# Kernel tuning notes

Measured on AMD Instinct MI355X. Metric: run time of the kernel, lower is better.

Reference implementation:

```python
import jax, jax.numpy as jnp
import numpy as np

C_LOGIT = 10.0  # logit clipping constant C from __init__
NEG_INF = -1e9


def setup_inputs() -> dict:
    key = jax.random.key(0)
    ks = jax.random.split(key, 12)
    B, S, E, H = 128, 1024, 128, 128
    sE = 1.0 / np.sqrt(E)
    s2E = 1.0 / np.sqrt(2 * E)
    return {
        "node_context": jnp.zeros((1,), jnp.float32),   # unused: low-decoder results are discarded
        "original_data": jnp.zeros((1,), jnp.float32),  # unused
        "cell_context": jax.random.normal(ks[0], (B, S, E), jnp.float32),
        "high_mask": jnp.zeros((B, S), jnp.float32),
        "low_mask": jnp.zeros((1,), jnp.float32),       # unused
        # learned parameters
        "init_w": jax.random.uniform(ks[1], (2 * E,), jnp.float32, -1.0, 1.0),
        "Wc": jax.random.uniform(ks[2], (E, E), jnp.float32, -sE, sE),    # h_context_embed
        "bc": jax.random.uniform(ks[3], (E,), jnp.float32, -sE, sE),
        "Wv": jax.random.uniform(ks[4], (2 * E, E), jnp.float32, -s2E, s2E),  # v_weight_embed
        "bv": jax.random.uniform(ks[5], (E,), jnp.float32, -s2E, s2E),
        "W_ref": jax.random.uniform(ks[6], (E, H), jnp.float32, -sE, sE),  # pointer target proj
        "W_q": jax.random.uniform(ks[7], (E, H), jnp.float32, -sE, sE),    # pointer query proj
        "v": jax.random.uniform(ks[8], (H,), jnp.float32, -1.0 / np.sqrt(H), 1.0 / np.sqrt(H)),
    }


def reference(node_context, original_data, cell_context, high_mask, low_mask,
              init_w, Wc, bc, Wv, bv, W_ref, W_q, v):
    B, S, E = cell_context.shape
    h_bar = jnp.mean(cell_context, axis=1) @ Wc + bc            # [B, E]
    ref = jnp.einsum('bse,eh->bsh', cell_context, W_ref)        # [B, S, H] (loop-invariant)
    q0 = h_bar + (init_w @ Wv + bv)                             # [B, E]
    mask0 = high_mask.at[:, 0].set(1.0)                         # start node masked
    base_key = jax.random.key(42)

    def step(carry, i):
        query, mask, init_h = carry
        q = query @ W_q                                         # [B, H]
        u = C_LOGIT * jnp.tanh(jnp.einsum('bsh,h->bs', jnp.tanh(ref + q[:, None, :]), v))
        logits = jnp.where(mask > 0, NEG_INF, u)                # [B, S]
        k = jax.random.fold_in(base_key, i)
        idx = jax.random.categorical(k, logits)                 # [B] sampled next node
        logp = jnp.take_along_axis(jax.nn.log_softmax(logits, -1), idx[:, None], 1)[:, 0]
        mask = mask.at[jnp.arange(B), idx].set(1.0)             # Environment.update_state
        h = jnp.take_along_axis(cell_context, idx[:, None, None], 1)[:, 0, :]  # gather emb
        init_h = jnp.where(i == 0, h, init_h)                   # frozen after first step
        query = h_bar + jnp.concatenate([init_h, h], axis=-1) @ Wv + bv
        return (query, mask, init_h), (logp, idx)

    init = (q0, mask0, jnp.zeros((B, E), cell_context.dtype))
    _, (logps, idxs) = jax.lax.scan(step, init, jnp.arange(S - 1))
    # original returns (stack(log_probs, 1), stack(idx, 1))
    return logps.T, idxs.T
```

## Files before the change

kernel.cpp:

```cpp
#include <hip/hip_runtime.h>
#include <hip/hip_bf16.h>
#include <stdint.h>

#pragma clang fp contract(off)

#define Bn 128
#define Sn 1024
#define En 128
#define NSTEP 1023
#define REQ_WS ((size_t)Bn * 128 * Sn * 4)

__device__ __forceinline__ uint2 threefry2x32(uint32_t k0, uint32_t k1,
                                              uint32_t x0, uint32_t x1) {
  uint32_t ks2 = k0 ^ k1 ^ 0x1BD11BDAu;
  x0 += k0; x1 += k1;
#define TFR(r) { x0 += x1; x1 = (x1 << (r)) | (x1 >> (32 - (r))); x1 ^= x0; }
  TFR(13) TFR(15) TFR(26) TFR(6)
  x0 += k1;  x1 += ks2 + 1u;
  TFR(17) TFR(29) TFR(16) TFR(24)
  x0 += ks2; x1 += k0 + 2u;
  TFR(13) TFR(15) TFR(26) TFR(6)
  x0 += k0;  x1 += k1 + 3u;
  TFR(17) TFR(29) TFR(16) TFR(24)
  x0 += k1;  x1 += ks2 + 4u;
  TFR(13) TFR(15) TFR(26) TFR(6)
  x0 += ks2; x1 += k0 + 5u;
#undef TFR
  return make_uint2(x0, x1);
}

__device__ __forceinline__ float xla_tanh(float x) {
#pragma clang fp contract(off)
  float cx = fmaxf(-7.90531110763549805f, fminf(x, 7.90531110763549805f));
  float x2 = cx * cx;
  float nu = -2.76076847742355e-16f;
  nu = x2 * nu + 2.00018790482477e-13f;
  nu = x2 * nu + -8.60467152213735e-11f;
  nu = x2 * nu + 5.12229709037114e-08f;
  nu = x2 * nu + 1.48572235717979e-05f;
  nu = x2 * nu + 6.37261928875436e-04f;
  nu = x2 * nu + 4.89352455891786e-03f;
  nu = cx * nu;
  float de = 1.19825839466702e-06f;
  de = x2 * de + 1.18534705686654e-04f;
  de = x2 * de + 2.26843463243900e-03f;
  de = x2 * de + 4.89352518554385e-03f;
  float r = nu / de;
  return (fabsf(x) < 0.0004f) ? x : r;
}

__device__ __forceinline__ float cephes_logf(float x) {
#pragma clang fp contract(off)
  uint32_t ix = __float_as_uint(x);
  int e = (int)(ix >> 23) - 126;
  float m = __uint_as_float((ix & 0x007FFFFFu) | 0x3F000000u);
  if (m < 0.70710678118654752440f) { e -= 1; m = m + m; }
  float xm = m - 1.0f;
  float z = xm * xm;
  float y = 7.0376836292e-2f;
  y = y * xm + -1.1514610310e-1f;
  y = y * xm + 1.1676998740e-1f;
  y = y * xm + -1.2420140846e-1f;
  y = y * xm + 1.4249322787e-1f;
  y = y * xm + -1.6668057665e-1f;
  y = y * xm + 2.0000714765e-1f;
  y = y * xm + -2.4999993993e-1f;
  y = y * xm + 3.3333331174e-1f;
  y = y * xm;
  y = y * z;
  float fe = (float)e;
  y = y + fe * -2.12194440e-4f;
  y = y - 0.5f * z;
  float res = xm + y;
  res = res + fe * 0.693359375f;
  return res;
}

__device__ __forceinline__ float cephes_expf(float x) {
#pragma clang fp contract(off)
  x = fminf(fmaxf(x, -88.3762626647949f), 88.3762626647950f);
  float fx = x * 1.44269504088896341f + 0.5f;
  fx = floorf(fx);
  x = x - fx * 0.693359375f;
  x = x - fx * -2.12194440e-4f;
  float z = x * x;
  float y = 1.9875691500e-4f;
  y = y * x + 1.3981999507e-3f;
  y = y * x + 8.3334519073e-3f;
  y = y * x + 4.1665795894e-2f;
  y = y * x + 1.6666665459e-1f;
  y = y * x + 5.0000001201e-1f;
  y = y * z + x;
  y = y + 1.0f;
  return ldexpf(y, (int)fx);
}

__device__ __forceinline__ uint32_t f32_orderable(float f) {
  uint32_t b = __float_as_uint(f);
  return (b & 0x80000000u) ? ~b : (b | 0x80000000u);
}

__global__ void k_mark(float* out, float val) { out[0] = val; }

__global__ __launch_bounds__(256) void k_ref(const float* __restrict__ cc,
    const float* __restrict__ W_ref, float* __restrict__ refT) {
#pragma clang fp contract(off)
  int b = blockIdx.y, s0 = blockIdx.x * 128, t = threadIdx.x;
  __shared__ float tile[128 * 129];
  const float* src = cc + ((size_t)b * Sn + s0) * En;
  for (int i = t; i < 128 * 128; i += 256) {
    int sl = i >> 7, e = i & 127;
    tile[sl * 129 + e] = src[i];
  }
  __syncthreads();
  for (int i = t; i < 128 * 128; i += 256) {
    int sl = i >> 7, h = i & 127;
    float acc = 0.0f;
    for (int e = 0; e < En; ++e)
      acc = acc + tile[sl * 129 + e] * W_ref[e * 128 + h];
    refT[((size_t)b * Sn + (s0 + sl)) * 128 + h] = acc;
  }
}

__global__ __launch_bounds__(1024) void k_decode(
    const float* __restrict__ cc, const float* __restrict__ high_mask,
    const float* __restrict__ init_w, const float* __restrict__ Wc,
    const float* __restrict__ bc, const float* __restrict__ Wv,
    const float* __restrict__ bv, const float* __restrict__ W_q,
    const float* __restrict__ v, const float* __restrict__ refT,
    float* __restrict__ out, int half) {
#pragma clang fp contract(off)
  const int b = blockIdx.x, tid = threadIdx.x;
  const int lane = tid & 63, wid = tid >> 6;
  const int hsel = tid & 1;
  __shared__ __align__(16) float wq_s[128 * 128];
  __shared__ __align__(16) float wvhi_s[128 * 128];
  __shared__ __align__(16) float mean_s[128], q_s[128], query_s[128], hbar_s[128];
  __shared__ __align__(16) float v_s[128], bv_s[128], cvec[256], dlow_s[128];
  __shared__ float uv[1024];
  __shared__ unsigned short list_s[1024];
  __shared__ unsigned long long wkey[16];
  __shared__ float wsum[16];
  __shared__ int n_s, p_s;
  __shared__ uint32_t key_s[2];

  for (int j = tid; j < 128 * 128; j += 1024) wq_s[j] = W_q[j];
  for (int j = tid; j < 128 * 128; j += 1024) wvhi_s[j] = Wv[128 * 128 + j];
  if (tid < 128) {
    float acc = 0.0f;
    const float* base = cc + (size_t)b * Sn * En + tid;
    for (int s = 0; s < Sn; ++s) acc = acc + base[(size_t)s * En];
    mean_s[tid] = acc / 1024.0f;
  }
  if (tid == 512) {
    int n = 0;
    for (int s = 0; s < Sn; ++s) {
      bool masked = (s == 0) || (high_mask[(size_t)b * Sn + s] > 0.0f);
      if (!masked) list_s[n++] = (unsigned short)s;
    }
    n_s = n;
  }
  __syncthreads();
  if (tid < 128) {
    float hb = 0.0f;
    for (int e = 0; e < 128; ++e) hb = hb + mean_s[e] * Wc[e * 128 + tid];
    hb = hb + bc[tid];
    float wd = 0.0f;
    for (int k = 0; k < 256; ++k) wd = wd + init_w[k] * Wv[k * 128 + tid];
    wd = wd + bv[tid];
    hbar_s[tid] = hb;
    query_s[tid] = hb + wd;
    v_s[tid] = v[tid];
    bv_s[tid] = bv[tid];
  }
  __syncthreads();

  const float* refb = refT + (size_t)b * Sn * 128;
  const float4* q4 = (const float4*)q_s;
  const float4* v4 = (const float4*)v_s;

  for (int i = 0; i < NSTEP; ++i) {
    const int n = n_s;
    if (tid < 128) {
      float acc = 0.0f;
#pragma unroll 8
      for (int k = 0; k < 128; ++k) acc = acc + query_s[k] * wq_s[k * 128 + tid];
      q_s[tid] = acc;
    } else if (tid == 512) {
      uint2 kk2 = threefry2x32(0u, 42u, 0u, (uint32_t)i);
      key_s[0] = kk2.x; key_s[1] = kk2.y;
    }
    __syncthreads();

    const int npass = (2 * n + 1023) >> 10;
    unsigned long long kk = 0ull;
    float ee = 0.0f;
    for (int pass = 0; pass < npass; ++pass) {
      const int row = (pass << 9) + (tid >> 1);
      if (row < n) {
        const int s = list_s[row];
        const float4* rb4 = (const float4*)(refb + (size_t)s * 128);
        float4 rA[8];
#pragma unroll
        for (int j = 0; j < 8; ++j) rA[j] = rb4[2 * j + hsel];
        float a0 = 0.f, a1 = 0.f, a2 = 0.f, a3 = 0.f;
        float4 rB[8];
#pragma unroll
        for (int c2 = 0; c2 < 8; ++c2) {
          rB[c2] = rb4[2 * (c2 + 8) + hsel];
          const float4 qv = q4[2 * c2 + hsel];
          const float4 vv = v4[2 * c2 + hsel];
          const float4 r = rA[c2];
          a0 = a0 + xla_tanh(r.x + qv.x) * vv.x;
          a1 = a1 + xla_tanh(r.y + qv.y) * vv.y;
          a2 = a2 + xla_tanh(r.z + qv.z) * vv.z;
          a3 = a3 + xla_tanh(r.w + qv.w) * vv.w;
        }
#pragma unroll
        for (int c2 = 8; c2 < 16; ++c2) {
          const float4 qv = q4[2 * c2 + hsel];
          const float4 vv = v4[2 * c2 + hsel];
          const float4 r = rB[c2 - 8];
          a0 = a0 + xla_tanh(r.x + qv.x) * vv.x;
          a1 = a1 + xla_tanh(r.y + qv.y) * vv.y;
          a2 = a2 + xla_tanh(r.z + qv.z) * vv.z;
          a3 = a3 + xla_tanh(r.w + qv.w) * vv.w;
        }
        float o0 = __shfl_xor(a0, 1, 64), o1 = __shfl_xor(a1, 1, 64);
        float o2 = __shfl_xor(a2, 1, 64), o3 = __shfl_xor(a3, 1, 64);
        if (hsel == 0) {
          float h0 = a0 + o0, h1 = a1 + o1, h2 = a2 + o2, h3 = a3 + o3;
          float dot = (h0 + h2) + (h1 + h3);
          float u = 10.0f * xla_tanh(dot);
          uint32_t f = (uint32_t)(b * Sn + s);
          uint2 hh = threefry2x32(key_s[0], key_s[1], 0u, f);
          uint32_t bits = hh.x ^ hh.y;
          float uf = __uint_as_float((bits >> 9) | 0x3F800000u) - 1.0f;
          uf = uf + 1.17549435e-38f;
          uf = fmaxf(1.17549435e-38f, uf);
          float g = -cephes_logf(-cephes_logf(uf));
          float y = u + g;
          uv[row] = u;
          unsigned long long k2 =
              ((unsigned long long)f32_orderable(y) << 32) | (uint32_t)(0xFFFFFFFFu - (uint32_t)row);
          if (k2 > kk) kk = k2;
          ee = ee + cephes_expf(u);
        }
      }
    }
    for (int off = 32; off >= 1; off >>= 1) {
      unsigned long long o = __shfl_xor(kk, off, 64);
      if (o > kk) kk = o;
      ee = ee + __shfl_xor(ee, off, 64);
    }
    if (lane == 0) { wkey[wid] = kk; wsum[wid] = ee; }
    __syncthreads();

    if (tid < 64) {
      unsigned long long k = (tid < 16) ? wkey[tid] : 0ull;
      float e = (tid < 16) ? wsum[tid] : 0.0f;
      for (int off = 8; off >= 1; off >>= 1) {
        unsigned long long o = __shfl_xor(k, off, 16);
        if (o > k) k = o;
        e = e + __shfl_xor(e, off, 16);
      }
      if (tid == 0) {
        int p = (int)(0xFFFFFFFFu - (uint32_t)(k & 0xFFFFFFFFu));
        p = (p >= 0 && p < 1024) ? p : 0;
        p_s = p;
        float logp = uv[p] - cephes_logf(e);
        out[(size_t)b * NSTEP + i] = logp;
        out[(size_t)half + (size_t)b * NSTEP + i] = (float)list_s[p];
        n_s = n - 1;
      }
    }
    __syncthreads();

    const int p = p_s;
    const int idx = list_s[p];
    unsigned short mv = 0;
    const bool doshift = (tid >= p) && (tid < n - 1);
    if (doshift) mv = list_s[tid + 1];
    if (tid < 128) {
      float hval = cc[((size_t)b * Sn + idx) * En + tid];
      cvec[128 + tid] = hval;
      if (i == 0) cvec[tid] = hval;
    }
    __syncthreads();

    if (doshift) list_s[tid] = mv;
    if (tid < 128) {
      float d;
      if (i == 0) {
        float dl = 0.0f;
#pragma unroll 8
        for (int k = 0; k < 128; ++k) dl = dl + cvec[k] * Wv[k * 128 + tid];
        dlow_s[tid] = dl;
        d = dl;
      } else {
        d = dlow_s[tid];
      }
#pragma unroll 8
      for (int k = 0; k < 128; ++k) d = d + cvec[128 + k] * wvhi_s[k * 128 + tid];
      query_s[tid] = (hbar_s[tid] + d) + bv_s[tid];
    }
    __syncthreads();
  }
}

extern "C" void kernel_launch(void* const* d_in, const int* in_sizes, int n_in,
                              void* d_out, int out_size, void* d_ws, size_t ws_size,
                              hipStream_t stream) {
  const float* cc     = (const float*)d_in[2];
  const float* hm     = (const float*)d_in[3];
  const float* init_w = (const float*)d_in[5];
  const float* Wc     = (const float*)d_in[6];
  const float* bc     = (const float*)d_in[7];
  const float* Wv     = (const float*)d_in[8];
  const float* bv     = (const float*)d_in[9];
  const float* W_ref  = (const float*)d_in[10];
  const float* W_q    = (const float*)d_in[11];
  const float* v      = (const float*)d_in[12];
  float* out = (float*)d_out;

  if (ws_size < REQ_WS) {
    float mib = (float)(ws_size >> 20);
    hipLaunchKernelGGL(k_mark, dim3(1), dim3(1), 0, stream, out, 100000.0f * (mib + 1.0f));
    return;
  }

  float* refT = (float*)d_ws;
  const int half = out_size / 2;

  hipLaunchKernelGGL(k_ref, dim3(Sn / 128, Bn), dim3(256), 0, stream, cc, W_ref, refT);
  hipLaunchKernelGGL(k_decode, dim3(Bn), dim3(1024), 0, stream,
                     cc, hm, init_w, Wc, bc, Wv, bv, W_q, v, refT, out, half);
}
```

Measured before the change: 22.00 ms.

## Double-buffer candidate list, redundant per-thread reduction, and prefetch ref rows

Replaces the single-thread final reduction and its broadcast barrier with every thread reducing the 16 wave partials redundantly from shared memory. The candidate list is double-buffered so compaction can be written in the same phase, which removes one __syncthreads per step. The first half of each thread's ref row is also loaded before the q projection so memory latency overlaps that work. The trade-off is extra shared-memory reads per thread, more shared memory for the second list, and higher register pressure from the prefetched row.

After: 35.07 ms. +59.4%, slower.

```diff
diff --git a/kernel.cpp b/kernel.cpp
--- a/kernel.cpp
+++ b/kernel.cpp
@@ -133,15 +133,16 @@
   const int b = blockIdx.x, tid = threadIdx.x;
   const int lane = tid & 63, wid = tid >> 6;
   const int hsel = tid & 1;
+  const int row1 = tid >> 1;
   __shared__ __align__(16) float wq_s[128 * 128];
   __shared__ __align__(16) float wvhi_s[128 * 128];
   __shared__ __align__(16) float mean_s[128], q_s[128], query_s[128], hbar_s[128];
   __shared__ __align__(16) float v_s[128], bv_s[128], cvec[256], dlow_s[128];
   __shared__ float uv[1024];
-  __shared__ unsigned short list_s[1024];
+  __shared__ unsigned short list2[2][1024];
   __shared__ unsigned long long wkey[16];
   __shared__ float wsum[16];
-  __shared__ int n_s, p_s;
+  __shared__ int n_s;
   __shared__ uint32_t key_s[2];
 
   for (int j = tid; j < 128 * 128; j += 1024) wq_s[j] = W_q[j];
@@ -156,7 +157,7 @@
     int n = 0;
     for (int s = 0; s < Sn; ++s) {
       bool masked = (s == 0) || (high_mask[(size_t)b * Sn + s] > 0.0f);
-      if (!masked) list_s[n++] = (unsigned short)s;
+      if (!masked) list2[0][n++] = (unsigned short)s;
     }
     n_s = n;
   }
@@ -174,13 +175,24 @@
     bv_s[tid] = bv[tid];
   }
   __syncthreads();
+  const int n0 = n_s;
 
   const float* refb = refT + (size_t)b * Sn * 128;
   const float4* q4 = (const float4*)q_s;
   const float4* v4 = (const float4*)v_s;
 
   for (int i = 0; i < NSTEP; ++i) {
-    const int n = n_s;
+    const int n = n0 - i;
+    const unsigned short* lcur = list2[i & 1];
+    unsigned short* lnxt = list2[(i + 1) & 1];
+
+    float4 rA[8];
+    const bool act1 = (row1 < n);
+    if (act1) {
+      const float4* rb4 = (const float4*)(refb + (size_t)lcur[row1] * 128);
+#pragma unroll
+      for (int j = 0; j < 8; ++j) rA[j] = rb4[2 * j + hsel];
+    }
     if (tid < 128) {
       float acc = 0.0f;
 #pragma unroll 8
@@ -196,31 +208,26 @@
     unsigned long long kk = 0ull;
     float ee = 0.0f;
     for (int pass = 0; pass < npass; ++pass) {
-      const int row = (pass << 9) + (tid >> 1);
+      const int row = (pass << 9) + row1;
       if (row < n) {
-        const int s = list_s[row];
+        const int s = lcur[row];
         const float4* rb4 = (const float4*)(refb + (size_t)s * 128);
-        float4 rA[8];
-#pragma unroll
-        for (int j = 0; j < 8; ++j) rA[j] = rb4[2 * j + hsel];
+        float4 rv[16];
+#pragma unroll
+        for (int j = 8; j < 16; ++j) rv[j] = rb4[2 * j + hsel];
+        if (pass == 0) {
+#pragma unroll
+          for (int j = 0; j < 8; ++j) rv[j] = rA[j];
+        } else {
+#pragma unroll
+          for (int j = 0; j < 8; ++j) rv[j] = rb4[2 * j + hsel];
+        }
         float a0 = 0.f, a1 = 0.f, a2 = 0.f, a3 = 0.f;
-        float4 rB[8];
-#pragma unroll
-        for (int c2 = 0; c2 < 8; ++c2) {
-          rB[c2] = rb4[2 * (c2 + 8) + hsel];
+#pragma unroll
+        for (int c2 = 0; c2 < 16; ++c2) {
           const float4 qv = q4[2 * c2 + hsel];
           const float4 vv = v4[2 * c2 + hsel];
-          const float4 r = rA[c2];
-          a0 = a0 + xla_tanh(r.x + qv.x) * vv.x;
-          a1 = a1 + xla_tanh(r.y + qv.y) * vv.y;
-          a2 = a2 + xla_tanh(r.z + qv.z) * vv.z;
-          a3 = a3 + xla_tanh(r.w + qv.w) * vv.w;
-        }
-#pragma unroll
-        for (int c2 = 8; c2 < 16; ++c2) {
-          const float4 qv = q4[2 * c2 + hsel];
-          const float4 vv = v4[2 * c2 + hsel];
-          const float4 r = rB[c2 - 8];
+          const float4 r = rv[c2];
           a0 = a0 + xla_tanh(r.x + qv.x) * vv.x;
           a1 = a1 + xla_tanh(r.y + qv.y) * vv.y;
           a2 = a2 + xla_tanh(r.z + qv.z) * vv.z;
@@ -256,39 +263,28 @@
     if (lane == 0) { wkey[wid] = kk; wsum[wid] = ee; }
     __syncthreads();
 
-    if (tid < 64) {
-      unsigned long long k = (tid < 16) ? wkey[tid] : 0ull;
-      float e = (tid < 16) ? wsum[tid] : 0.0f;
-      for (int off = 8; off >= 1; off >>= 1) {
-        unsigned long long o = __shfl_xor(k, off, 16);
-        if (o > k) k = o;
-        e = e + __shfl_xor(e, off, 16);
-      }
-      if (tid == 0) {
-        int p = (int)(0xFFFFFFFFu - (uint32_t)(k & 0xFFFFFFFFu));
-        p = (p >= 0 && p < 1024) ? p : 0;
-        p_s = p;
-        float logp = uv[p] - cephes_logf(e);
-        out[(size_t)b * NSTEP + i] = logp;
-        out[(size_t)half + (size_t)b * NSTEP + i] = (float)list_s[p];
-        n_s = n - 1;
-      }
-    }
-    __syncthreads();
-
-    const int p = p_s;
-    const int idx = list_s[p];
-    unsigned short mv = 0;
-    const bool doshift = (tid >= p) && (tid < n - 1);
-    if (doshift) mv = list_s[tid + 1];
+    unsigned long long km = wkey[0];
+    float es = wsum[0];
+    for (int w = 1; w < 16; ++w) {
+      if (wkey[w] > km) km = wkey[w];
+      es = es + wsum[w];
+    }
+    int p = (int)(0xFFFFFFFFu - (uint32_t)(km & 0xFFFFFFFFu));
+    p = (p >= 0 && p < 1024) ? p : 0;
+    const int idx = lcur[p];
     if (tid < 128) {
       float hval = cc[((size_t)b * Sn + idx) * En + tid];
       cvec[128 + tid] = hval;
       if (i == 0) cvec[tid] = hval;
     }
+    if (tid < n - 1) lnxt[tid] = lcur[tid + (tid >= p ? 1 : 0)];
+    if (tid == 0) {
+      float logp = uv[p] - cephes_logf(es);
+      out[(size_t)b * NSTEP + i] = logp;
+      out[(size_t)half + (size_t)b * NSTEP + i] = (float)idx;
+    }
     __syncthreads();
 
-    if (doshift) list_s[tid] = mv;
     if (tid < 128) {
       float d;
       if (i == 0) {
```
